# Optimization experiments

Hardware: AMD Instinct MI355X
Metric: run time of the kernel (lower is better)

The kernel has to match this reference:

```python
import jax, jax.numpy as jnp
import numpy as np

CUTOFF = 10.0
NUM_GAUSSIANS = 50
LOG2 = float(np.log(2.0))
PI = float(np.pi)


def ssp(v):
    # shifted softplus: softplus(x) - log(2)
    return jax.nn.softplus(v) - LOG2


def setup_inputs() -> dict:
    key = jax.random.key(0)
    ks = jax.random.split(key, 16)
    N, E, H, F, G, L = 10000, 320000, 128, 128, NUM_GAUSSIANS, 6
    s = 0.08  # param scale to keep activations stable over 6 layers
    return {
        "x": jax.random.randint(ks[0], (N,), 0, 100),
        "edge_index": jax.random.randint(ks[1], (2, E), 0, N),
        "edge_dist": jax.random.uniform(ks[2], (E,), jnp.float32) * CUTOFF,
        "emb": jax.random.normal(ks[3], (100, H), jnp.float32) * s,
        "mlp_w1": jax.random.normal(ks[4], (L, G, F), jnp.float32) * s,
        "mlp_b1": jnp.zeros((L, F), jnp.float32),
        "mlp_w2": jax.random.normal(ks[5], (L, F, F), jnp.float32) * s,
        "mlp_b2": jnp.zeros((L, F), jnp.float32),
        "lin1_w": jax.random.normal(ks[6], (L, H, F), jnp.float32) * s,
        "lin2_w": jax.random.normal(ks[7], (L, F, H), jnp.float32) * s,
        "lin2_b": jnp.zeros((L, H), jnp.float32),
        "lin_w": jax.random.normal(ks[8], (L, H, H), jnp.float32) * s,
        "lin_b": jnp.zeros((L, H), jnp.float32),
        "out1_w": jax.random.normal(ks[9], (H, H // 2), jnp.float32) * s,
        "out1_b": jnp.zeros((H // 2,), jnp.float32),
        "out2_w": jax.random.normal(ks[10], (H // 2, H // 2), jnp.float32) * s,
        "out2_b": jnp.zeros((H // 2,), jnp.float32),
        "ro_w": jax.random.normal(ks[11], (H // 2, 12), jnp.float32) * s,
        "ro_b": jnp.zeros((12,), jnp.float32),
    }


def reference(x, edge_index, edge_dist, emb, mlp_w1, mlp_b1, mlp_w2, mlp_b2,
              lin1_w, lin2_w, lin2_b, lin_w, lin_b,
              out1_w, out1_b, out2_w, out2_b, ro_w, ro_b):
    N = x.shape[0]
    L = mlp_w1.shape[0]
    src, dst = edge_index[0], edge_index[1]

    h = emb[x]  # [N, H]

    # Gaussian smearing of distances -> [E, G]
    offset = jnp.linspace(0.0, CUTOFF, NUM_GAUSSIANS)
    coeff = -0.5 / (offset[1] - offset[0]) ** 2
    ea = jnp.exp(coeff * (edge_dist[:, None] - offset[None, :]) ** 2)

    # cosine cutoff envelope C [E]
    C = 0.5 * (jnp.cos(edge_dist * PI / CUTOFF) + 1.0)

    for l in range(L):
        # per-edge filter: MLP(gaussian) * cutoff  -> [E, F]
        W = (ssp(ea @ mlp_w1[l] + mlp_b1[l]) @ mlp_w2[l] + mlp_b2[l]) * C[:, None]
        xf = h @ lin1_w[l]                      # [N, F] (lin1, no bias)
        msg = xf[src] * W                       # gather + elementwise [E, F]
        agg = jax.ops.segment_sum(msg, dst, num_segments=N)  # scatter-add
        conv = agg @ lin2_w[l] + lin2_b[l]      # [N, H]
        h = h + (ssp(conv) @ lin_w[l] + lin_b[l])

    t = ssp(h @ out1_w + out1_b)
    t = t @ out2_w + out2_b
    h_agg = jnp.sum(t, axis=0)                  # [H//2]
    return h_agg @ ro_w + ro_b                  # [12]
```

## Files before the change

### kernel.cpp

```cpp
#include <hip/hip_runtime.h>
#include <math.h>

#define E_NUM 320000
#define N_NUM 10000
#define NB8   (N_NUM / 8)
#define NB16  (N_NUM / 16)
#define TAB   2048

typedef unsigned short ushort_t;
typedef short short8_t __attribute__((ext_vector_type(8)));
typedef float f32x4    __attribute__((ext_vector_type(4)));

#define WP_O1   294912
#define WP_O2   303104
#define WP_W1T  307200
#define WP_W2T  356352
#define WP_TOT  454656

__device__ __forceinline__ float ssp_f(float x) {
    return fmaxf(x, 0.f) + __logf(1.f + __expf(-fabsf(x))) - 0.69314718056f;
}

__device__ __forceinline__ float bf2f(ushort_t u) {
    union { unsigned int i; float f; } v;
    v.i = ((unsigned int)u) << 16;
    return v.f;
}
__device__ __forceinline__ ushort_t f2bf(float f) {
    union { float f; unsigned int i; } v;
    v.f = f;
    unsigned int u = v.i;
    unsigned int r = (u + 0x7FFFu + ((u >> 16) & 1u)) >> 16;
    return (ushort_t)r;
}

__global__ __launch_bounds__(256) void hist_kernel(const int* __restrict__ ei,
                                                   int* __restrict__ counts) {
    int e = blockIdx.x * 256 + threadIdx.x;
    if (e < E_NUM) atomicAdd(&counts[ei[E_NUM + e]], 1);
}

__global__ __launch_bounds__(256) void scan_kernel(const int* __restrict__ counts,
                                                   int* __restrict__ offs,
                                                   int* __restrict__ cursor) {
    __shared__ int part[256];
    const int tid = threadIdx.x;
    const int CH = 40;
    int base = tid * CH;
    int s = 0;
    for (int i = 0; i < CH; ++i) {
        int idx = base + i;
        if (idx < N_NUM) s += counts[idx];
    }
    part[tid] = s;
    __syncthreads();
    for (int off = 1; off < 256; off <<= 1) {
        int v = (tid >= off) ? part[tid - off] : 0;
        __syncthreads();
        part[tid] += v;
        __syncthreads();
    }
    int run = (tid > 0) ? part[tid - 1] : 0;
    for (int i = 0; i < CH; ++i) {
        int idx = base + i;
        if (idx < N_NUM) {
            offs[idx] = run;
            cursor[idx] = run;
            run += counts[idx];
        }
    }
    if (tid == 255) offs[N_NUM] = part[255];
}

__global__ __launch_bounds__(256) void scatter_kernel(const int* __restrict__ ei,
                                                      const float* __restrict__ dist,
                                                      int* __restrict__ cursor,
                                                      int* __restrict__ meta) {
    int e = blockIdx.x * 256 + threadIdx.x;
    if (e >= E_NUM) return;
    int d = ei[E_NUM + e];
    int pos = atomicAdd(&cursor[d], 1);
    float t = dist[e] * ((float)(TAB - 1) / 10.0f);
    int i0 = (int)(t + 0.5f);
    if (i0 > TAB - 1) i0 = TAB - 1;
    meta[pos] = (i0 << 14) | ei[e];
}

__global__ __launch_bounds__(256) void pack_kernel(const float* __restrict__ lin2_w,
                                                   const float* __restrict__ lin_w,
                                                   const float* __restrict__ lin1_w,
                                                   const float* __restrict__ o1w,
                                                   const float* __restrict__ o2w,
                                                   const float* __restrict__ mlp_w1,
                                                   const float* __restrict__ mlp_w2,
                                                   short* __restrict__ wpack) {
    int idx = blockIdx.x * 256 + threadIdx.x;
    const int M128 = 16384;
    if (idx < 18 * M128) {
        int g = idx / M128, r = idx % M128;
        const float* src;
        if (g < 6) src = lin2_w + g * M128;
        else if (g < 12) src = lin_w + (g - 6) * M128;
        else src = lin1_w + (g - 12) * M128;
        int j = r & 7, L = (r >> 3) & 63, ks = (r >> 9) & 3, t = r >> 11;
        int n = t * 16 + (L & 15);
        int k = ks * 32 + (L >> 4) * 8 + j;
        wpack[idx] = (short)f2bf(src[k * 128 + n]);
    } else if (idx < WP_O2) {
        int r = idx - WP_O1;
        int j = r & 7, L = (r >> 3) & 63, ks = (r >> 9) & 3, t = r >> 11;
        int n = t * 16 + (L & 15);
        int k = ks * 32 + (L >> 4) * 8 + j;
        wpack[idx] = (short)f2bf(o1w[k * 64 + n]);
    } else if (idx < WP_W1T) {
        int r = idx - WP_O2;
        int j = r & 7, L = (r >> 3) & 63, ks = (r >> 9) & 1, t = r >> 10;
        int n = t * 16 + (L & 15);
        int k = ks * 32 + (L >> 4) * 8 + j;
        wpack[idx] = (short)f2bf(o2w[k * 64 + n]);
    } else if (idx < WP_W2T) {
        int r2 = idx - WP_W1T;
        int g = r2 / 8192, r = r2 % 8192;
        int j = r & 7, L = (r >> 3) & 63, ks = (r >> 9) & 1, t = r >> 10;
        int n = t * 16 + (L & 15);
        int k = ks * 32 + (L >> 4) * 8 + j;
        float v = (k < 50) ? mlp_w1[g * 6400 + k * 128 + n] : 0.f;
        wpack[idx] = (short)f2bf(v);
    } else if (idx < WP_TOT) {
        int r2 = idx - WP_W2T;
        int g = r2 / M128, r = r2 % M128;
        int j = r & 7, L = (r >> 3) & 63, ks = (r >> 9) & 3, t = r >> 11;
        int n = t * 16 + (L & 15);
        int k = ks * 32 + (L >> 4) * 8 + j;
        wpack[idx] = (short)f2bf(mlp_w2[g * M128 + k * 128 + n]);
    }
}

__global__ __launch_bounds__(512) void table_kernel(const short* __restrict__ w1t,
                                                    const float* __restrict__ mlp_b1,
                                                    const short* __restrict__ w2t,
                                                    const float* __restrict__ mlp_b2,
                                                    ushort_t* __restrict__ tabB) {
    __shared__ short EA[16 * 72];
    __shared__ short HD[16 * 136];
    const int tid = threadIdx.x;
    const int wv = tid >> 6;
    const int lane = tid & 63;
    const int l = blockIdx.x >> 7;
    const int r0 = (blockIdx.x & 127) * 16;
    const float DG = 10.0f / (float)(TAB - 1);
    const float STEP = 10.0f / 49.0f;
    const float COEFF = -0.5f / (STEP * STEP);

    for (int i = tid; i < 16 * 64; i += 512) {
        int r = i >> 6, k = i & 63;
        float v = 0.f;
        if (k < 50) {
            float d = (float)(r0 + r) * DG;
            float t = d - (float)k * STEP;
            v = __expf(COEFF * t * t);
        }
        EA[r * 72 + k] = (short)f2bf(v);
    }
    __syncthreads();

    const int m = lane & 15, q = lane >> 4;

    {
        f32x4 acc = {0.f, 0.f, 0.f, 0.f};
        #pragma unroll
        for (int ks = 0; ks < 2; ++ks) {
            short8_t a = *(const short8_t*)(EA + m * 72 + ks * 32 + q * 8);
            short8_t b = *(const short8_t*)(w1t + l * 8192 + (wv * 2 + ks) * 512 + lane * 8);
            acc = __builtin_amdgcn_mfma_f32_16x16x32_bf16(a, b, acc, 0, 0, 0);
        }
        float bv = mlp_b1[l * 128 + wv * 16 + m];
        #pragma unroll
        for (int i = 0; i < 4; ++i)
            HD[(q * 4 + i) * 136 + wv * 16 + m] = (short)f2bf(ssp_f(acc[i] + bv));
    }
    __syncthreads();

    {
        f32x4 acc = {0.f, 0.f, 0.f, 0.f};
        #pragma unroll
        for (int ks = 0; ks < 4; ++ks) {
            short8_t a = *(const short8_t*)(HD + m * 136 + ks * 32 + q * 8);
            short8_t b = *(const short8_t*)(w2t + l * 16384 + (wv * 4 + ks) * 512 + lane * 8);
            acc = __builtin_amdgcn_mfma_f32_16x16x32_bf16(a, b, acc, 0, 0, 0);
        }
        int col = wv * 16 + m;
        float bv = mlp_b2[l * 128 + col];
        ushort_t* tl = tabB + (size_t)l * TAB * 128;
        #pragma unroll
        for (int i = 0; i < 4; ++i) {
            int row = r0 + q * 4 + i;
            float d = (float)row * DG;
            float C = 0.5f * (__cosf(d * 0.31415926535f) + 1.0f);
            tl[(size_t)row * 128 + col] = f2bf((acc[i] + bv) * C);
        }
    }
}

__device__ __forceinline__ void nacc8(short8_t x, short8_t t, float* o) {
    #pragma unroll
    for (int j = 0; j < 8; ++j)
        o[j] = fmaf(bf2f((ushort_t)x[j]), bf2f((ushort_t)t[j]), o[j]);
}

__global__ __launch_bounds__(256) void embed_lin1_kernel(const int* __restrict__ x,
                                                         const float* __restrict__ emb,
                                                         const float* __restrict__ B,
                                                         float* __restrict__ h,
                                                         ushort_t* __restrict__ xf) {
    __shared__ float AT[128][9];
    __shared__ int s_x[8];
    const int tid = threadIdx.x;
    const int n0 = blockIdx.x * 8;

    if (tid < 8) s_x[tid] = x[n0 + tid];
    __syncthreads();
    for (int i = tid; i < 8 * 128; i += 256) {
        int r = i >> 7, c = i & 127;
        float v = emb[s_x[r] * 128 + c];
        AT[c][r] = v;
        h[(size_t)(n0 + r) * 128 + c] = v;
    }
    __syncthreads();

    const int r  = tid & 7;
    const int c0 = (tid >> 3) * 4;
    float acc[4] = {0.f, 0.f, 0.f, 0.f};
    for (int k = 0; k < 128; k += 4) {
        float a[4];
        #pragma unroll
        for (int u = 0; u < 4; ++u) a[u] = AT[k + u][r];
        #pragma unroll
        for (int u = 0; u < 4; ++u) {
            float4 b = *(const float4*)(B + (size_t)(k + u) * 128 + c0);
            acc[0] = fmaf(a[u], b.x, acc[0]);
            acc[1] = fmaf(a[u], b.y, acc[1]);
            acc[2] = fmaf(a[u], b.z, acc[2]);
            acc[3] = fmaf(a[u], b.w, acc[3]);
        }
    }
    ushort4 o;
    o.x = f2bf(acc[0]); o.y = f2bf(acc[1]); o.z = f2bf(acc[2]); o.w = f2bf(acc[3]);
    *(ushort4*)(xf + (size_t)(n0 + r) * 128 + c0) = o;
}

__device__ __forceinline__ void mfma_stage2(const short* A_lds, const short* wp,
                                            int lane, int t0, int t1,
                                            f32x4& acc0, f32x4& acc1) {
    const int m = lane & 15, q = lane >> 4;
    #pragma unroll
    for (int ks = 0; ks < 4; ++ks) {
        short8_t a  = *(const short8_t*)(A_lds + m * 136 + ks * 32 + q * 8);
        short8_t b0 = *(const short8_t*)(wp + (t0 * 4 + ks) * 512 + lane * 8);
        short8_t b1 = *(const short8_t*)(wp + (t1 * 4 + ks) * 512 + lane * 8);
        acc0 = __builtin_amdgcn_mfma_f32_16x16x32_bf16(a, b0, acc0, 0, 0, 0);
        acc1 = __builtin_amdgcn_mfma_f32_16x16x32_bf16(a, b1, acc1, 0, 0, 0);
    }
}

template <bool LAST>
__global__ __launch_bounds__(256) void layer_kernel(const int* __restrict__ offs,
                                                    const int* __restrict__ meta,
                                                    const ushort_t* __restrict__ xf,
                                                    const ushort_t* __restrict__ tabB,
                                                    const short* __restrict__ w2p,
                                                    const float* __restrict__ lin2_b,
                                                    const short* __restrict__ wlp,
                                                    const float* __restrict__ lin_b,
                                                    const short* __restrict__ w1p,
                                                    float* __restrict__ h,
                                                    ushort_t* __restrict__ xf_out,
                                                    const short* __restrict__ o1p,
                                                    const float* __restrict__ o1b,
                                                    const short* __restrict__ o2p,
                                                    const float* __restrict__ o2b,
                                                    float* __restrict__ gs) {
    __shared__ short A1[16 * 136];
    __shared__ short A2[16 * 136];
    __shared__ float red[4][64];
    const int tid = threadIdx.x;
    const int n0 = blockIdx.x * 16;
    const int wv = tid >> 6;
    const int lane = tid & 63;

    {
        const int qt = lane >> 4;
        const int c8 = (lane & 15) * 8;
        const int node = n0 + wv * 4 + qt;
        int e   = offs[node];
        int end = offs[node + 1];

        float accA[8] = {0.f, 0.f, 0.f, 0.f, 0.f, 0.f, 0.f, 0.f};
        float accB[8] = {0.f, 0.f, 0.f, 0.f, 0.f, 0.f, 0.f, 0.f};

        for (; e + 8 <= end; e += 8) {
            int m[8];
            #pragma unroll
            for (int u = 0; u < 8; ++u) m[u] = meta[e + u];
            short8_t xv[8], tv[8];
            #pragma unroll
            for (int u = 0; u < 8; ++u) {
                xv[u] = *(const short8_t*)(xf + (size_t)(m[u] & 0x3FFF) * 128 + c8);
                tv[u] = *(const short8_t*)(tabB + (size_t)((unsigned)m[u] >> 14) * 128 + c8);
            }
            #pragma unroll
            for (int u = 0; u < 8; ++u)
                nacc8(xv[u], tv[u], (u & 1) ? accB : accA);
        }
        for (; e + 4 <= end; e += 4) {
            int m[4];
            #pragma unroll
            for (int u = 0; u < 4; ++u) m[u] = meta[e + u];
            short8_t xv[4], tv[4];
            #pragma unroll
            for (int u = 0; u < 4; ++u) {
                xv[u] = *(const short8_t*)(xf + (size_t)(m[u] & 0x3FFF) * 128 + c8);
                tv[u] = *(const short8_t*)(tabB + (size_t)((unsigned)m[u] >> 14) * 128 + c8);
            }
            #pragma unroll
            for (int u = 0; u < 4; ++u)
                nacc8(xv[u], tv[u], (u & 1) ? accB : accA);
        }
        for (; e < end; ++e) {
            int mm = meta[e];
            short8_t xv = *(const short8_t*)(xf + (size_t)(mm & 0x3FFF) * 128 + c8);
            short8_t tv = *(const short8_t*)(tabB + (size_t)((unsigned)mm >> 14) * 128 + c8);
            nacc8(xv, tv, accA);
        }

        short8_t out;
        #pragma unroll
        for (int j = 0; j < 8; ++j) out[j] = (short)f2bf(accA[j] + accB[j]);
        *(short8_t*)&A1[(wv * 4 + qt) * 136 + c8] = out;
    }
    __syncthreads();

    const int m = lane & 15, q = lane >> 4;
    const int t0 = wv * 2, t1 = wv * 2 + 1;

    {
        f32x4 acc0 = {0.f, 0.f, 0.f, 0.f}, acc1 = {0.f, 0.f, 0.f, 0.f};
        mfma_stage2(A1, w2p, lane, t0, t1, acc0, acc1);
        float bv0 = lin2_b[t0 * 16 + m];
        float bv1 = lin2_b[t1 * 16 + m];
        #pragma unroll
        for (int i = 0; i < 4; ++i) {
            int r = q * 4 + i;
            A2[r * 136 + t0 * 16 + m] = (short)f2bf(ssp_f(acc0[i] + bv0));
            A2[r * 136 + t1 * 16 + m] = (short)f2bf(ssp_f(acc1[i] + bv1));
        }
    }
    __syncthreads();

    {
        f32x4 acc0 = {0.f, 0.f, 0.f, 0.f}, acc1 = {0.f, 0.f, 0.f, 0.f};
        mfma_stage2(A2, wlp, lane, t0, t1, acc0, acc1);
        float bv0 = lin_b[t0 * 16 + m];
        float bv1 = lin_b[t1 * 16 + m];
        #pragma unroll
        for (int i = 0; i < 4; ++i) {
            int r = q * 4 + i;
            int grow = n0 + r;
            float h0 = h[(size_t)grow * 128 + t0 * 16 + m];
            float h1 = h[(size_t)grow * 128 + t1 * 16 + m];
            float hn0 = h0 + acc0[i] + bv0;
            float hn1 = h1 + acc1[i] + bv1;
            if (!LAST) {
                h[(size_t)grow * 128 + t0 * 16 + m] = hn0;
                h[(size_t)grow * 128 + t1 * 16 + m] = hn1;
            }
            A1[r * 136 + t0 * 16 + m] = (short)f2bf(hn0);
            A1[r * 136 + t1 * 16 + m] = (short)f2bf(hn1);
        }
    }
    __syncthreads();

    if constexpr (!LAST) {
        f32x4 acc0 = {0.f, 0.f, 0.f, 0.f}, acc1 = {0.f, 0.f, 0.f, 0.f};
        mfma_stage2(A1, w1p, lane, t0, t1, acc0, acc1);
        #pragma unroll
        for (int i = 0; i < 4; ++i) {
            int r = q * 4 + i;
            int grow = n0 + r;
            xf_out[(size_t)grow * 128 + t0 * 16 + m] = f2bf(acc0[i]);
            xf_out[(size_t)grow * 128 + t1 * 16 + m] = f2bf(acc1[i]);
        }
    } else {
        {
            f32x4 acc = {0.f, 0.f, 0.f, 0.f};
            #pragma unroll
            for (int ks = 0; ks < 4; ++ks) {
                short8_t a = *(const short8_t*)(A1 + m * 136 + ks * 32 + q * 8);
                short8_t b = *(const short8_t*)(o1p + (wv * 4 + ks) * 512 + lane * 8);
                acc = __builtin_amdgcn_mfma_f32_16x16x32_bf16(a, b, acc, 0, 0, 0);
            }
            float bv = o1b[wv * 16 + m];
            #pragma unroll
            for (int i = 0; i < 4; ++i) {
                int r = q * 4 + i;
                A2[r * 136 + wv * 16 + m] = (short)f2bf(ssp_f(acc[i] + bv));
            }
        }
        __syncthreads();
        {
            f32x4 acc = {0.f, 0.f, 0.f, 0.f};
            #pragma unroll
            for (int ks = 0; ks < 2; ++ks) {
                short8_t a = *(const short8_t*)(A2 + m * 136 + ks * 32 + q * 8);
                short8_t b = *(const short8_t*)(o2p + (wv * 2 + ks) * 512 + lane * 8);
                acc = __builtin_amdgcn_mfma_f32_16x16x32_bf16(a, b, acc, 0, 0, 0);
            }
            float bv = o2b[wv * 16 + m];
            float part = acc[0] + acc[1] + acc[2] + acc[3] + 4.0f * bv;
            red[q][wv * 16 + m] = part;
        }
        __syncthreads();
        if (tid < 64) {
            float s = red[0][tid] + red[1][tid] + red[2][tid] + red[3][tid];
            atomicAdd(&gs[tid], s);
        }
    }
}

__global__ void final_kernel(const float* __restrict__ gs,
                             const float* __restrict__ ro_w,
                             const float* __restrict__ ro_b,
                             float* __restrict__ out) {
    int i = threadIdx.x;
    if (i < 12) {
        float s = ro_b[i];
        for (int k = 0; k < 64; ++k) s = fmaf(gs[k], ro_w[k * 12 + i], s);
        out[i] = s;
    }
}

extern "C" void kernel_launch(void* const* d_in, const int* in_sizes, int n_in,
                              void* d_out, int out_size, void* d_ws, size_t ws_size,
                              hipStream_t stream) {
    const int*   x      = (const int*)d_in[0];
    const int*   ei     = (const int*)d_in[1];
    const float* dist   = (const float*)d_in[2];
    const float* emb    = (const float*)d_in[3];
    const float* mlp_w1 = (const float*)d_in[4];
    const float* mlp_b1 = (const float*)d_in[5];
    const float* mlp_w2 = (const float*)d_in[6];
    const float* mlp_b2 = (const float*)d_in[7];
    const float* lin1_w = (const float*)d_in[8];
    const float* lin2_w = (const float*)d_in[9];
    const float* lin2_b = (const float*)d_in[10];
    const float* lin_w  = (const float*)d_in[11];
    const float* lin_b  = (const float*)d_in[12];
    const float* out1_w = (const float*)d_in[13];
    const float* out1_b = (const float*)d_in[14];
    const float* out2_w = (const float*)d_in[15];
    const float* out2_b = (const float*)d_in[16];
    const float* ro_w   = (const float*)d_in[17];
    const float* ro_b   = (const float*)d_in[18];
    float* out = (float*)d_out;

    char* base = (char*)d_ws;
    float*    h     = (float*)base;     base += (size_t)N_NUM * 128 * 4;
    ushort_t* tabB  = (ushort_t*)base;  base += (size_t)6 * TAB * 128 * 2;
    ushort_t* xf0   = (ushort_t*)base;  base += (size_t)N_NUM * 128 * 2;
    ushort_t* xf1   = (ushort_t*)base;  base += (size_t)N_NUM * 128 * 2;
    int*      meta  = (int*)base;       base += (size_t)E_NUM * 4;
    short*    wpack = (short*)base;     base += (size_t)WP_TOT * 2;
    float*    gs    = (float*)base;     base += 64 * 4;
    int*      offs  = (int*)base;       base += (N_NUM + 1) * 4;
    int*      cursor= (int*)base;       base += N_NUM * 4;
    int*      counts= (int*)base;       base += N_NUM * 4;

    hipMemsetAsync(counts, 0, N_NUM * sizeof(int), stream);
    hipMemsetAsync(gs, 0, 64 * sizeof(float), stream);

    hist_kernel<<<(E_NUM + 255) / 256, 256, 0, stream>>>(ei, counts);
    scan_kernel<<<1, 256, 0, stream>>>(counts, offs, cursor);
    scatter_kernel<<<(E_NUM + 255) / 256, 256, 0, stream>>>(ei, dist, cursor, meta);

    pack_kernel<<<(WP_TOT + 255) / 256, 256, 0, stream>>>(
        lin2_w, lin_w, lin1_w, out1_w, out2_w, mlp_w1, mlp_w2, wpack);
    table_kernel<<<6 * (TAB / 16), 512, 0, stream>>>(
        wpack + WP_W1T, mlp_b1, wpack + WP_W2T, mlp_b2, tabB);

    embed_lin1_kernel<<<NB8, 256, 0, stream>>>(x, emb, lin1_w, h, xf0);

    const short* o1p = wpack + WP_O1;
    const short* o2p = wpack + WP_O2;

    for (int l = 0; l < 6; ++l) {
        ushort_t* xin  = (l & 1) ? xf1 : xf0;
        ushort_t* xout = (l & 1) ? xf0 : xf1;
        const ushort_t* tl = tabB + (size_t)l * TAB * 128;
        const short* w2p = wpack + l * 16384;
        const short* wlp = wpack + (6 + l) * 16384;
        if (l < 5) {
            const short* w1p = wpack + (12 + l + 1) * 16384;
            layer_kernel<false><<<NB16, 256, 0, stream>>>(
                offs, meta, xin, tl,
                w2p, lin2_b + l * 128, wlp, lin_b + l * 128, w1p,
                h, xout, nullptr, nullptr, nullptr, nullptr, nullptr);
        } else {
            layer_kernel<true><<<NB16, 256, 0, stream>>>(
                offs, meta, xin, tl,
                w2p, lin2_b + l * 128, wlp, lin_b + l * 128, nullptr,
                h, nullptr, o1p, out1_b, o2p, out2_b, gs);
        }
    }

    final_kernel<<<1, 64, 0, stream>>>(gs, ro_w, ro_b, out);
}
```

Baseline: 322.7 us.

## Split edge aggregation across two wave groups and fuse setup kernels

Layer kernels now launch 512 threads per 16-node block. Two wave groups each aggregate half of every node's edge range, and the partial sums are combined through shared memory. Each MFMA stage now gives one 16-column tile per wave instead of two. Setup kernels are merged: histogram with weight packing, and scatter with embedding/lin1. The scan is widened to 1024 threads. The aim is more parallelism on the gather-bound aggregation and fewer launches, at the cost of an extra barrier and shared-memory buffer per layer.

```diff
diff --git a/kernel.cpp b/kernel.cpp
--- a/kernel.cpp
+++ b/kernel.cpp
@@ -16,6 +16,10 @@
 #define WP_W1T  307200
 #define WP_W2T  356352
 #define WP_TOT  454656
+
+#define HB  1250
+#define PB  ((WP_TOT + 255) / 256)
+#define SCB 1250
 
 __device__ __forceinline__ float ssp_f(float x) {
     return fmaxf(x, 0.f) + __logf(1.f + __expf(-fabsf(x))) - 0.69314718056f;
@@ -34,67 +38,22 @@
     return (ushort_t)r;
 }
 
-__global__ __launch_bounds__(256) void hist_kernel(const int* __restrict__ ei,
-                                                   int* __restrict__ counts) {
-    int e = blockIdx.x * 256 + threadIdx.x;
-    if (e < E_NUM) atomicAdd(&counts[ei[E_NUM + e]], 1);
-}
-
-__global__ __launch_bounds__(256) void scan_kernel(const int* __restrict__ counts,
-                                                   int* __restrict__ offs,
-                                                   int* __restrict__ cursor) {
-    __shared__ int part[256];
-    const int tid = threadIdx.x;
-    const int CH = 40;
-    int base = tid * CH;
-    int s = 0;
-    for (int i = 0; i < CH; ++i) {
-        int idx = base + i;
-        if (idx < N_NUM) s += counts[idx];
-    }
-    part[tid] = s;
-    __syncthreads();
-    for (int off = 1; off < 256; off <<= 1) {
-        int v = (tid >= off) ? part[tid - off] : 0;
-        __syncthreads();
-        part[tid] += v;
-        __syncthreads();
-    }
-    int run = (tid > 0) ? part[tid - 1] : 0;
-    for (int i = 0; i < CH; ++i) {
-        int idx = base + i;
-        if (idx < N_NUM) {
-            offs[idx] = run;
-            cursor[idx] = run;
-            run += counts[idx];
-        }
-    }
-    if (tid == 255) offs[N_NUM] = part[255];
-}
-
-__global__ __launch_bounds__(256) void scatter_kernel(const int* __restrict__ ei,
-                                                      const float* __restrict__ dist,
-                                                      int* __restrict__ cursor,
-                                                      int* __restrict__ meta) {
-    int e = blockIdx.x * 256 + threadIdx.x;
-    if (e >= E_NUM) return;
-    int d = ei[E_NUM + e];
-    int pos = atomicAdd(&cursor[d], 1);
-    float t = dist[e] * ((float)(TAB - 1) / 10.0f);
-    int i0 = (int)(t + 0.5f);
-    if (i0 > TAB - 1) i0 = TAB - 1;
-    meta[pos] = (i0 << 14) | ei[e];
-}
-
-__global__ __launch_bounds__(256) void pack_kernel(const float* __restrict__ lin2_w,
-                                                   const float* __restrict__ lin_w,
-                                                   const float* __restrict__ lin1_w,
-                                                   const float* __restrict__ o1w,
-                                                   const float* __restrict__ o2w,
-                                                   const float* __restrict__ mlp_w1,
-                                                   const float* __restrict__ mlp_w2,
-                                                   short* __restrict__ wpack) {
-    int idx = blockIdx.x * 256 + threadIdx.x;
+__global__ __launch_bounds__(256) void hist_pack_kernel(const int* __restrict__ ei,
+                                                        int* __restrict__ counts,
+                                                        const float* __restrict__ lin2_w,
+                                                        const float* __restrict__ lin_w,
+                                                        const float* __restrict__ lin1_w,
+                                                        const float* __restrict__ o1w,
+                                                        const float* __restrict__ o2w,
+                                                        const float* __restrict__ mlp_w1,
+                                                        const float* __restrict__ mlp_w2,
+                                                        short* __restrict__ wpack) {
+    if (blockIdx.x < HB) {
+        int e = blockIdx.x * 256 + threadIdx.x;
+        if (e < E_NUM) atomicAdd(&counts[ei[E_NUM + e]], 1);
+        return;
+    }
+    int idx = (blockIdx.x - HB) * 256 + threadIdx.x;
     const int M128 = 16384;
     if (idx < 18 * M128) {
         int g = idx / M128, r = idx % M128;
@@ -136,6 +95,96 @@
     }
 }
 
+__global__ __launch_bounds__(1024) void scan_kernel(const int* __restrict__ counts,
+                                                    int* __restrict__ offs,
+                                                    int* __restrict__ cursor) {
+    __shared__ int part[1024];
+    const int tid = threadIdx.x;
+    const int CH = 10;
+    int base = tid * CH;
+    int s = 0;
+    #pragma unroll
+    for (int i = 0; i < CH; ++i) {
+        int idx = base + i;
+        if (idx < N_NUM) s += counts[idx];
+    }
+    part[tid] = s;
+    __syncthreads();
+    for (int off = 1; off < 1024; off <<= 1) {
+        int v = (tid >= off) ? part[tid - off] : 0;
+        __syncthreads();
+        part[tid] += v;
+        __syncthreads();
+    }
+    int run = (tid > 0) ? part[tid - 1] : 0;
+    #pragma unroll
+    for (int i = 0; i < CH; ++i) {
+        int idx = base + i;
+        if (idx < N_NUM) {
+            offs[idx] = run;
+            cursor[idx] = run;
+            run += counts[idx];
+        }
+    }
+    if (tid == 1023) offs[N_NUM] = part[1023];
+}
+
+__global__ __launch_bounds__(256) void scatter_embed_kernel(const int* __restrict__ ei,
+                                                            const float* __restrict__ dist,
+                                                            int* __restrict__ cursor,
+                                                            int* __restrict__ meta,
+                                                            const int* __restrict__ x,
+                                                            const float* __restrict__ emb,
+                                                            const float* __restrict__ B,
+                                                            float* __restrict__ h,
+                                                            ushort_t* __restrict__ xf) {
+    if (blockIdx.x < SCB) {
+        int e = blockIdx.x * 256 + threadIdx.x;
+        if (e >= E_NUM) return;
+        int d = ei[E_NUM + e];
+        int pos = atomicAdd(&cursor[d], 1);
+        float t = dist[e] * ((float)(TAB - 1) / 10.0f);
+        int i0 = (int)(t + 0.5f);
+        if (i0 > TAB - 1) i0 = TAB - 1;
+        meta[pos] = (i0 << 14) | ei[e];
+        return;
+    }
+    __shared__ float AT[128][9];
+    __shared__ int s_x[8];
+    const int tid = threadIdx.x;
+    const int n0 = (blockIdx.x - SCB) * 8;
+
+    if (tid < 8) s_x[tid] = x[n0 + tid];
+    __syncthreads();
+    for (int i = tid; i < 8 * 128; i += 256) {
+        int r = i >> 7, c = i & 127;
+        float v = emb[s_x[r] * 128 + c];
+        AT[c][r] = v;
+        h[(size_t)(n0 + r) * 128 + c] = v;
+    }
+    __syncthreads();
+
+    const int r  = tid & 7;
+    const int c0 = (tid >> 3) * 4;
+    float acc[4] = {0.f, 0.f, 0.f, 0.f};
+    for (int k = 0; k < 128; k += 4) {
+        float a[4];
+        #pragma unroll
+        for (int u = 0; u < 4; ++u) a[u] = AT[k + u][r];
+        #pragma unroll
+        for (int u = 0; u < 4; ++u) {
+            float4 b = *(const float4*)(B + (size_t)(k + u) * 128 + c0);
+            acc[0] = fmaf(a[u], b.x, acc[0]);
+            acc[1] = fmaf(a[u], b.y, acc[1]);
+            acc[2] = fmaf(a[u], b.z, acc[2]);
+            acc[3] = fmaf(a[u], b.w, acc[3]);
+        }
+    }
+    ushort4 o;
+    o.x = f2bf(acc[0]); o.y = f2bf(acc[1]); o.z = f2bf(acc[2]); o.w = f2bf(acc[3]);
+    *(ushort4*)(xf + (size_t)(n0 + r) * 128 + c0) = o;
+}
+
 __global__ __launch_bounds__(512) void table_kernel(const short* __restrict__ w1t,
                                                     const float* __restrict__ mlp_b1,
                                                     const short* __restrict__ w2t,
@@ -208,63 +257,8 @@
         o[j] = fmaf(bf2f((ushort_t)x[j]), bf2f((ushort_t)t[j]), o[j]);
 }
 
-__global__ __launch_bounds__(256) void embed_lin1_kernel(const int* __restrict__ x,
-                                                         const float* __restrict__ emb,
-                                                         const float* __restrict__ B,
-                                                         float* __restrict__ h,
-                                                         ushort_t* __restrict__ xf) {
-    __shared__ float AT[128][9];
-    __shared__ int s_x[8];
-    const int tid = threadIdx.x;
-    const int n0 = blockIdx.x * 8;
-
-    if (tid < 8) s_x[tid] = x[n0 + tid];
-    __syncthreads();
-    for (int i = tid; i < 8 * 128; i += 256) {
-        int r = i >> 7, c = i & 127;
-        float v = emb[s_x[r] * 128 + c];
-        AT[c][r] = v;
-        h[(size_t)(n0 + r) * 128 + c] = v;
-    }
-    __syncthreads();
-
-    const int r  = tid & 7;
-    const int c0 = (tid >> 3) * 4;
-    float acc[4] = {0.f, 0.f, 0.f, 0.f};
-    for (int k = 0; k < 128; k += 4) {
-        float a[4];
-        #pragma unroll
-        for (int u = 0; u < 4; ++u) a[u] = AT[k + u][r];
-        #pragma unroll
-        for (int u = 0; u < 4; ++u) {
-            float4 b = *(const float4*)(B + (size_t)(k + u) * 128 + c0);
-            acc[0] = fmaf(a[u], b.x, acc[0]);
-            acc[1] = fmaf(a[u], b.y, acc[1]);
-            acc[2] = fmaf(a[u], b.z, acc[2]);
-            acc[3] = fmaf(a[u], b.w, acc[3]);
-        }
-    }
-    ushort4 o;
-    o.x = f2bf(acc[0]); o.y = f2bf(acc[1]); o.z = f2bf(acc[2]); o.w = f2bf(acc[3]);
-    *(ushort4*)(xf + (size_t)(n0 + r) * 128 + c0) = o;
-}
-
-__device__ __forceinline__ void mfma_stage2(const short* A_lds, const short* wp,
-                                            int lane, int t0, int t1,
-                                            f32x4& acc0, f32x4& acc1) {
-    const int m = lane & 15, q = lane >> 4;
-    #pragma unroll
-    for (int ks = 0; ks < 4; ++ks) {
-        short8_t a  = *(const short8_t*)(A_lds + m * 136 + ks * 32 + q * 8);
-        short8_t b0 = *(const short8_t*)(wp + (t0 * 4 + ks) * 512 + lane * 8);
-        short8_t b1 = *(const short8_t*)(wp + (t1 * 4 + ks) * 512 + lane * 8);
-        acc0 = __builtin_amdgcn_mfma_f32_16x16x32_bf16(a, b0, acc0, 0, 0, 0);
-        acc1 = __builtin_amdgcn_mfma_f32_16x16x32_bf16(a, b1, acc1, 0, 0, 0);
-    }
-}
-
 template <bool LAST>
-__global__ __launch_bounds__(256) void layer_kernel(const int* __restrict__ offs,
+__global__ __launch_bounds__(512) void layer_kernel(const int* __restrict__ offs,
                                                     const int* __restrict__ meta,
                                                     const ushort_t* __restrict__ xf,
                                                     const ushort_t* __restrict__ tabB,
@@ -282,18 +276,24 @@
                                                     float* __restrict__ gs) {
     __shared__ short A1[16 * 136];
     __shared__ short A2[16 * 136];
+    __shared__ float P[16 * 128];
     __shared__ float red[4][64];
     const int tid = threadIdx.x;
     const int n0 = blockIdx.x * 16;
     const int wv = tid >> 6;
     const int lane = tid & 63;
+    const int strm = wv >> 2;
 
     {
         const int qt = lane >> 4;
         const int c8 = (lane & 15) * 8;
-        const int node = n0 + wv * 4 + qt;
-        int e   = offs[node];
-        int end = offs[node + 1];
+        const int row = (wv & 3) * 4 + qt;
+        const int node = n0 + row;
+        int s0 = offs[node];
+        int s1 = offs[node + 1];
+        int mid = s0 + ((s1 - s0) >> 1);
+        int e   = strm ? mid : s0;
+        int end = strm ? s1  : mid;
 
         float accA[8] = {0.f, 0.f, 0.f, 0.f, 0.f, 0.f, 0.f, 0.f};
         float accB[8] = {0.f, 0.f, 0.f, 0.f, 0.f, 0.f, 0.f, 0.f};
@@ -333,65 +333,77 @@
             nacc8(xv, tv, accA);
         }
 
-        short8_t out;
-        #pragma unroll
-        for (int j = 0; j < 8; ++j) out[j] = (short)f2bf(accA[j] + accB[j]);
-        *(short8_t*)&A1[(wv * 4 + qt) * 136 + c8] = out;
+        if (!strm) {
+            #pragma unroll
+            for (int j = 0; j < 8; ++j)
+                P[row * 128 + c8 + j] = accA[j] + accB[j];
+        }
+        __syncthreads();
+        if (strm) {
+            short8_t out;
+            #pragma unroll
+            for (int j = 0; j < 8; ++j)
+                out[j] = (short)f2bf(accA[j] + accB[j] + P[row * 128 + c8 + j]);
+            *(short8_t*)&A1[row * 136 + c8] = out;
+        }
     }
     __syncthreads();
 
     const int m = lane & 15, q = lane >> 4;
-    const int t0 = wv * 2, t1 = wv * 2 + 1;
+    const int t = wv;
 
     {
-        f32x4 acc0 = {0.f, 0.f, 0.f, 0.f}, acc1 = {0.f, 0.f, 0.f, 0.f};
-        mfma_stage2(A1, w2p, lane, t0, t1, acc0, acc1);
-        float bv0 = lin2_b[t0 * 16 + m];
-        float bv1 = lin2_b[t1 * 16 + m];
-        #pragma unroll
-        for (int i = 0; i < 4; ++i) {
-            int r = q * 4 + i;
-            A2[r * 136 + t0 * 16 + m] = (short)f2bf(ssp_f(acc0[i] + bv0));
-            A2[r * 136 + t1 * 16 + m] = (short)f2bf(ssp_f(acc1[i] + bv1));
-        }
+        f32x4 acc = {0.f, 0.f, 0.f, 0.f};
+        #pragma unroll
+        for (int ks = 0; ks < 4; ++ks) {
+            short8_t a = *(const short8_t*)(A1 + m * 136 + ks * 32 + q * 8);
+            short8_t b = *(const short8_t*)(w2p + (t * 4 + ks) * 512 + lane * 8);
+            acc = __builtin_amdgcn_mfma_f32_16x16x32_bf16(a, b, acc, 0, 0, 0);
+        }
+        float bv = lin2_b[t * 16 + m];
+        #pragma unroll
+        for (int i = 0; i < 4; ++i)
+            A2[(q * 4 + i) * 136 + t * 16 + m] = (short)f2bf(ssp_f(acc[i] + bv));
     }
     __syncthreads();
 
     {
-        f32x4 acc0 = {0.f, 0.f, 0.f, 0.f}, acc1 = {0.f, 0.f, 0.f, 0.f};
-        mfma_stage2(A2, wlp, lane, t0, t1, acc0, acc1);
-        float bv0 = lin_b[t0 * 16 + m];
-        float bv1 = lin_b[t1 * 16 + m];
+        f32x4 acc = {0.f, 0.f, 0.f, 0.f};
+        #pragma unroll
+        for (int ks = 0; ks < 4; ++ks) {
+            short8_t a = *(const short8_t*)(A2 + m * 136 + ks * 32 + q * 8);
+            short8_t b = *(const short8_t*)(wlp + (t * 4 + ks) * 512 + lane * 8);
+            acc = __builtin_amdgcn_mfma_f32_16x16x32_bf16(a, b, acc, 0, 0, 0);
+        }
+        float bv = lin_b[t * 16 + m];
         #pragma unroll
         for (int i = 0; i < 4; ++i) {
             int r = q * 4 + i;
             int grow = n0 + r;
-            float h0 = h[(size_t)grow * 128 + t0 * 16 + m];
-            float h1 = h[(size_t)grow * 128 + t1 * 16 + m];
-            float hn0 = h0 + acc0[i] + bv0;
-            float hn1 = h1 + acc1[i] + bv1;
-            if (!LAST) {
-                h[(size_t)grow * 128 + t0 * 16 + m] = hn0;
-                h[(size_t)grow * 128 + t1 * 16 + m] = hn1;
-            }
-            A1[r * 136 + t0 * 16 + m] = (short)f2bf(hn0);
-            A1[r * 136 + t1 * 16 + m] = (short)f2bf(hn1);
+            float h0 = h[(size_t)grow * 128 + t * 16 + m];
+            float hn = h0 + acc[i] + bv;
+            if (!LAST) h[(size_t)grow * 128 + t * 16 + m] = hn;
+            A1[r * 136 + t * 16 + m] = (short)f2bf(hn);
         }
     }
     __syncthreads();
 
     if constexpr (!LAST) {
-        f32x4 acc0 = {0.f, 0.f, 0.f, 0.f}, acc1 = {0.f, 0.f, 0.f, 0.f};
-        mfma_stage2(A1, w1p, lane, t0, t1, acc0, acc1);
+        f32x4 acc = {0.f, 0.f, 0.f, 0.f};
+        #pragma unroll
+        for (int ks = 0; ks < 4; ++ks) {
+            short8_t a = *(const short8_t*)(A1 + m * 136 + ks * 32 + q * 8);
+            short8_t b = *(const short8_t*)(w1p + (t * 4 + ks) * 512 + lane * 8);
+            acc = __builtin_amdgcn_mfma_f32_16x16x32_bf16(a, b, acc, 0, 0, 0);
+        }
         #pragma unroll
         for (int i = 0; i < 4; ++i) {
             int r = q * 4 + i;
             int grow = n0 + r;
-            xf_out[(size_t)grow * 128 + t0 * 16 + m] = f2bf(acc0[i]);
-            xf_out[(size_t)grow * 128 + t1 * 16 + m] = f2bf(acc1[i]);
+            xf_out[(size_t)grow * 128 + t * 16 + m] = f2bf(acc[i]);
         }
     } else {
-        {
+        if (wv < 4) {
             f32x4 acc = {0.f, 0.f, 0.f, 0.f};
             #pragma unroll
             for (int ks = 0; ks < 4; ++ks) {
@@ -407,7 +419,7 @@
             }
         }
         __syncthreads();
-        {
+        if (wv < 4) {
             f32x4 acc = {0.f, 0.f, 0.f, 0.f};
             #pragma unroll
             for (int ks = 0; ks < 2; ++ks) {
@@ -478,16 +490,16 @@
     hipMemsetAsync(counts, 0, N_NUM * sizeof(int), stream);
     hipMemsetAsync(gs, 0, 64 * sizeof(float), stream);
 
-    hist_kernel<<<(E_NUM + 255) / 256, 256, 0, stream>>>(ei, counts);
-    scan_kernel<<<1, 256, 0, stream>>>(counts, offs, cursor);
-    scatter_kernel<<<(E_NUM + 255) / 256, 256, 0, stream>>>(ei, dist, cursor, meta);
-
-    pack_kernel<<<(WP_TOT + 255) / 256, 256, 0, stream>>>(
-        lin2_w, lin_w, lin1_w, out1_w, out2_w, mlp_w1, mlp_w2, wpack);
+    hist_pack_kernel<<<HB + PB, 256, 0, stream>>>(
+        ei, counts, lin2_w, lin_w, lin1_w, out1_w, out2_w, mlp_w1, mlp_w2, wpack);
+
+    scan_kernel<<<1, 1024, 0, stream>>>(counts, offs, cursor);
+
+    scatter_embed_kernel<<<SCB + NB8, 256, 0, stream>>>(
+        ei, dist, cursor, meta, x, emb, lin1_w, h, xf0);
+
     table_kernel<<<6 * (TAB / 16), 512, 0, stream>>>(
         wpack + WP_W1T, mlp_b1, wpack + WP_W2T, mlp_b2, tabB);
-
-    embed_lin1_kernel<<<NB8, 256, 0, stream>>>(x, emb, lin1_w, h, xf0);
 
     const short* o1p = wpack + WP_O1;
     const short* o2p = wpack + WP_O2;
@@ -500,12 +512,12 @@
         const short* wlp = wpack + (6 + l) * 16384;
         if (l < 5) {
             const short* w1p = wpack + (12 + l + 1) * 16384;
-            layer_kernel<false><<<NB16, 256, 0, stream>>>(
+            layer_kernel<false><<<NB16, 512, 0, stream>>>(
                 offs, meta, xin, tl,
                 w2p, lin2_b + l * 128, wlp, lin_b + l * 128, w1p,
                 h, xout, nullptr, nullptr, nullptr, nullptr, nullptr);
         } else {
-            layer_kernel<true><<<NB16, 256, 0, stream>>>(
+            layer_kernel<true><<<NB16, 512, 0, stream>>>(
                 offs, meta, xin, tl,
                 w2p, lin2_b + l * 128, wlp, lin_b + l * 128, nullptr,
                 h, nullptr, o1p, out1_b, o2p, out2_b, gs);
```

After: 325.5 us. No clear change (+0.9%).
